# Kernel optimization log

Measured on AMD Instinct MI355X. Metric: run time of the kernel, lower is better.

Reference implementation:

```python
import jax, jax.numpy as jnp
import numpy as np

NUM_HEADS = 2
NUM_POINTS = 8
EMBED_DIM = 128


def conv2d(x, w, b, pad):
    # x: [B,C,H,W], w: [O,I,kh,kw]
    y = jax.lax.conv_general_dilated(
        x, w, window_strides=(1, 1), padding=[(pad, pad), (pad, pad)],
        dimension_numbers=('NCHW', 'OIHW', 'NCHW'))
    return y + b[None, :, None, None]


def grid_sample_bilinear(img, g):
    # img: [C,H,W]; g: [Ho,Wo,2] in [-1,1], (x, y) order; align_corners=False, zero padding
    C, H, W = img.shape
    x = ((g[..., 0] + 1.0) * W - 1.0) * 0.5
    y = ((g[..., 1] + 1.0) * H - 1.0) * 0.5
    x0 = jnp.floor(x); y0 = jnp.floor(y)
    x1 = x0 + 1.0; y1 = y0 + 1.0
    wx = x - x0; wy = y - y0

    def gather(yi, xi):
        valid = (xi >= 0) & (xi < W) & (yi >= 0) & (yi < H)
        xi_c = jnp.clip(xi, 0, W - 1).astype(jnp.int32)
        yi_c = jnp.clip(yi, 0, H - 1).astype(jnp.int32)
        v = img[:, yi_c, xi_c]  # [C,Ho,Wo]
        return v * valid[None].astype(img.dtype)

    out = (gather(y0, x0) * ((1 - wy) * (1 - wx))[None]
           + gather(y0, x1) * ((1 - wy) * wx)[None]
           + gather(y1, x0) * (wy * (1 - wx))[None]
           + gather(y1, x1) * (wy * wx)[None])
    return out  # [C,Ho,Wo]


def setup_inputs() -> dict:
    key = jax.random.key(0)
    ks = jax.random.split(key, 6)
    B, C, H, W = 8, EMBED_DIM, 96, 96
    query = jax.random.normal(ks[0], (B, C, H, W), dtype=jnp.float32)
    value = jax.random.normal(ks[1], (B, C, H, W), dtype=jnp.float32)
    reference_points = jax.random.uniform(ks[2], (B, H, W, NUM_HEADS, NUM_POINTS, 2), dtype=jnp.float32)
    attn_w = jax.random.normal(ks[3], (NUM_HEADS * NUM_POINTS, C, 3, 3), dtype=jnp.float32) * 0.05
    attn_b = jnp.zeros((NUM_HEADS * NUM_POINTS,), dtype=jnp.float32)
    proj_w = jax.random.normal(ks[4], (C, C, 1, 1), dtype=jnp.float32) * 0.05
    proj_b = jnp.zeros((C,), dtype=jnp.float32)
    return {"query": query, "value": value, "reference_points": reference_points,
            "attn_w": attn_w, "attn_b": attn_b, "proj_w": proj_w, "proj_b": proj_b}


def reference(query, value, reference_points, attn_w, attn_b, proj_w, proj_b):
    B, C, H, W = query.shape
    nh, npts = NUM_HEADS, NUM_POINTS
    hd = C // nh

    # attention weights: Conv2d(C, nh*np, 3, pad=1) -> softmax over points
    attn = conv2d(query, attn_w, attn_b, 1).reshape(B, nh, npts, H, W)
    attn = jax.nn.softmax(attn, axis=2)

    # grid: [B,H,W,nh,np,2] in [0,1] -> [-1,1] -> [B*nh, np, H, W, 2]
    grid = reference_points * 2.0 - 1.0
    grid = jnp.transpose(grid, (0, 3, 4, 1, 2, 5)).reshape(B * nh, npts, H, W, 2)

    # value per head: [B*nh, hd, H, W]
    val = value.reshape(B, nh, hd, H, W).reshape(B * nh, hd, H, W)

    # sample each point from the shared per-head value map (no materialized expand)
    sample_pts = jax.vmap(grid_sample_bilinear, in_axes=(None, 0))   # over points
    sampled = jax.vmap(sample_pts, in_axes=(0, 0))(val, grid)        # [B*nh, np, hd, H, W]
    sampled = sampled.reshape(B, nh, npts, hd, H, W)

    # weighted sum over points
    weighted = jnp.einsum('bnphw,bnpdhw->bndhw', attn, sampled).reshape(B, C, H, W)

    return conv2d(weighted, proj_w, proj_b, 0)
```

## Files before the change

### kernel.cpp

```cpp
#include <hip/hip_runtime.h>
#include <hip/hip_bf16.h>

#define BB 8
#define CC 128
#define HH 96
#define WW 96
#define HWH (HH*WW)
#define NH 2
#define NP 8
#define PW 98
#define PHW (PW*PW)

typedef __attribute__((ext_vector_type(8))) short short8;
typedef __attribute__((ext_vector_type(4))) float f32x4;

__device__ __forceinline__ float bf_lo(unsigned u) { return __uint_as_float(u << 16); }
__device__ __forceinline__ float bf_hi(unsigned u) { return __uint_as_float(u & 0xffff0000u); }

__global__ __launch_bounds__(256) void prep_w_kernel(
    const float* __restrict__ aw, const float* __restrict__ pw,
    __hip_bfloat16* __restrict__ wtb, float* __restrict__ pwT) {
  int t = blockIdx.x * 256 + threadIdx.x;
  for (int idx = t; idx < 9 * 16 * 16 * 8; idx += gridDim.x * 256) {
    int j = idx & 7;
    int o = (idx >> 3) & 15;
    int g = (idx >> 7) & 15;
    int k = idx >> 11;
    int c = g * 8 + j;
    wtb[idx] = __float2bfloat16(aw[o * 1152 + c * 9 + k]);
  }
  for (int idx = t; idx < 128 * 128; idx += gridDim.x * 256) {
    int co = idx & 127;
    int ci = idx >> 7;
    pwT[ci * 128 + co] = pw[co * 128 + ci];
  }
}

__global__ __launch_bounds__(256) void transpose_cl_kernel(
    const float* __restrict__ value, const float* __restrict__ query,
    __hip_bfloat16* __restrict__ val_t, __hip_bfloat16* __restrict__ q_pad) {
  __shared__ float tile[64][65];
  int blk = blockIdx.x;
  int mode = blk / 2304;
  int r = blk % 2304;
  int ptile = r % 144;
  int bn = r / 144;
  int b = bn >> 1, n = bn & 1;
  int pix0 = ptile * 64;
  int t = threadIdx.x;
  int lane = t & 63;
  int row4 = t >> 6;

  const float* srcp = (mode ? query : value) + ((size_t)(b * CC + n * 64)) * HWH + pix0;
#pragma unroll
  for (int i = 0; i < 16; ++i) {
    int c = i * 4 + row4;
    tile[c][lane] = srcp[(size_t)c * HWH + lane];
  }
  __syncthreads();

  int d2 = t & 31;
  int ph = t >> 5;
  if (mode == 0) {
    __hip_bfloat16* dst = val_t + ((size_t)bn * HWH + pix0) * 64;
#pragma unroll
    for (int i = 0; i < 8; ++i) {
      int p = i * 8 + ph;
      __hip_bfloat162 v;
      v.x = __float2bfloat16(tile[d2 * 2][p]);
      v.y = __float2bfloat16(tile[d2 * 2 + 1][p]);
      *reinterpret_cast<__hip_bfloat162*>(dst + (size_t)p * 64 + d2 * 2) = v;
    }
  } else {
#pragma unroll
    for (int i = 0; i < 8; ++i) {
      int p = i * 8 + ph;
      int gp = pix0 + p;
      int h = gp / WW, w = gp - h * WW;
      __hip_bfloat162 v;
      v.x = __float2bfloat16(tile[d2 * 2][p]);
      v.y = __float2bfloat16(tile[d2 * 2 + 1][p]);
      size_t off = ((size_t)b * PHW + (size_t)(h + 1) * PW + (w + 1)) * 128 + n * 64 + d2 * 2;
      *reinterpret_cast<__hip_bfloat162*>(q_pad + off) = v;
    }
  }
}

__global__ __launch_bounds__(256) void attn_conv_mfma2(
    const __hip_bfloat16* __restrict__ q_pad, const __hip_bfloat16* __restrict__ wtb_,
    const float* __restrict__ bias, float* __restrict__ attn_out) {
  int t = threadIdx.x;
  int l = t & 63;
  int bid = blockIdx.x;
  int sbid = (bid & 7) * 144 + (bid >> 3);
  int tid = __builtin_amdgcn_readfirstlane(sbid * 4 + (t >> 6));
  int b = tid / 576;
  int rem = tid % 576;
  int h = rem / 6;
  int w0 = (rem % 6) * 16;

  const char* qb = (const char*)q_pad;
  const char* wb = (const char*)wtb_;

  int pxbase = b * PHW + (h + 1) * PW + (w0 + 1);
  int lb  = (l & 15) * 256 + (l >> 4) * 16;
  int wlb = (l >> 4) * 256 + (l & 15) * 16;

  float bias_o = bias[l & 15];
  f32x4 acc0 = {bias_o, bias_o, bias_o, bias_o};
  f32x4 acc1 = {0.f, 0.f, 0.f, 0.f};

#pragma unroll
  for (int k = 0; k < 9; ++k) {
    int dy = k / 3 - 1, dx = (k % 3) - 1;
    const char* abase = qb + ((size_t)pxbase + dy * PW + dx) * 256 + lb;
    const char* bbase = wb + k * 4096 + wlb;
#pragma unroll
    for (int c4 = 0; c4 < 4; ++c4) {
      short8 a = *(const short8*)(abase + c4 * 64);
      short8 bf = *(const short8*)(bbase + c4 * 1024);
      if (k & 1)
        acc1 = __builtin_amdgcn_mfma_f32_16x16x32_bf16(a, bf, acc1, 0, 0, 0);
      else
        acc0 = __builtin_amdgcn_mfma_f32_16x16x32_bf16(a, bf, acc0, 0, 0, 0);
    }
  }

  int o = l & 15;
  size_t row0 = (size_t)b * HWH + (size_t)h * 96 + w0 + (l >> 4) * 4;
#pragma unroll
  for (int r = 0; r < 4; ++r) {
    float vv = acc0[r] + acc1[r];
    float mx = vv;
    mx = fmaxf(mx, __shfl_xor(mx, 1, 64));
    mx = fmaxf(mx, __shfl_xor(mx, 2, 64));
    mx = fmaxf(mx, __shfl_xor(mx, 4, 64));
    float e = __expf(vv - mx);
    float s = e;
    s += __shfl_xor(s, 1, 64);
    s += __shfl_xor(s, 2, 64);
    s += __shfl_xor(s, 4, 64);
    attn_out[(row0 + r) * 16 + o] = e / s;
  }
}

__global__ __launch_bounds__(256) void sample_kernel(
    const __hip_bfloat16* __restrict__ val_t, const float* __restrict__ attn,
    const float* __restrict__ refp, __hip_bfloat16* __restrict__ weighted) {
  int t = threadIdx.x;
  int lane = t & 63;
  int sub = lane >> 4;
  int lq = lane & 15;
  int bid = blockIdx.x;
  int sbid = (bid & 7) * 1152 + (bid >> 3);
  int unit = (sbid * 4 + (t >> 6)) * 4 + sub;
  int bn = unit / HWH;
  int pix = unit - bn * HWH;
  int bq = bn >> 1, n = bn & 1;

  const float* ap = attn + ((size_t)bq * HWH + pix) * 16 + n * 8;
  const float* rp = refp + (((size_t)bq * HWH + pix) * NH + n) * 16;
  const __hip_bfloat16* vb = val_t + (size_t)bn * (HWH * 64);

  float4 a0 = *(const float4*)(ap);
  float4 a1 = *(const float4*)(ap + 4);
  float4 r0 = *(const float4*)(rp);
  float4 r1 = *(const float4*)(rp + 4);
  float4 r2 = *(const float4*)(rp + 8);
  float4 r3 = *(const float4*)(rp + 12);
  float aa[8] = {a0.x, a0.y, a0.z, a0.w, a1.x, a1.y, a1.z, a1.w};
  float rr[16] = {r0.x, r0.y, r0.z, r0.w, r1.x, r1.y, r1.z, r1.w,
                  r2.x, r2.y, r2.z, r2.w, r3.x, r3.y, r3.z, r3.w};

  float acc0 = 0.f, acc1 = 0.f, acc2 = 0.f, acc3 = 0.f;
  int lq4 = lq * 4;
#pragma unroll
  for (int p = 0; p < 8; ++p) {
    float a = aa[p];
    float x = rr[p * 2 + 0] * (float)WW - 0.5f;
    float y = rr[p * 2 + 1] * (float)HH - 0.5f;
    float x0f = floorf(x), y0f = floorf(y);
    float wx = x - x0f, wy = y - y0f;
    int x0 = (int)x0f, y0 = (int)y0f;

    float ay0 = a * (1.f - wy);  ay0 = (y0 >= 0)      ? ay0 : 0.f;
    float ay1 = a * wy;          ay1 = (y0 < HH - 1)  ? ay1 : 0.f;
    float bx0 = 1.f - wx;        bx0 = (x0 >= 0)      ? bx0 : 0.f;
    float bx1 = wx;              bx1 = (x0 < WW - 1)  ? bx1 : 0.f;

    int xc0 = max(x0, 0), xc1 = min(x0 + 1, WW - 1);
    int yc0 = max(y0, 0), yc1 = min(y0 + 1, HH - 1);

    int r0o = yc0 * (WW * 64);
    int r1o = yc1 * (WW * 64);
    int c0o = xc0 * 64 + lq4;
    int c1o = xc1 * 64 + lq4;

    const uint2* p00 = (const uint2*)(vb + (r0o + c0o));
    const uint2* p01 = (const uint2*)(vb + (r0o + c1o));
    const uint2* p10 = (const uint2*)(vb + (r1o + c0o));
    const uint2* p11 = (const uint2*)(vb + (r1o + c1o));
    uint2 u00 = *p00, u01 = *p01, u10 = *p10, u11 = *p11;

    float w00 = ay0 * bx0, w01 = ay0 * bx1, w10 = ay1 * bx0, w11 = ay1 * bx1;

    acc0 = fmaf(bf_lo(u00.x), w00, acc0);
    acc1 = fmaf(bf_hi(u00.x), w00, acc1);
    acc2 = fmaf(bf_lo(u00.y), w00, acc2);
    acc3 = fmaf(bf_hi(u00.y), w00, acc3);

    acc0 = fmaf(bf_lo(u01.x), w01, acc0);
    acc1 = fmaf(bf_hi(u01.x), w01, acc1);
    acc2 = fmaf(bf_lo(u01.y), w01, acc2);
    acc3 = fmaf(bf_hi(u01.y), w01, acc3);

    acc0 = fmaf(bf_lo(u10.x), w10, acc0);
    acc1 = fmaf(bf_hi(u10.x), w10, acc1);
    acc2 = fmaf(bf_lo(u10.y), w10, acc2);
    acc3 = fmaf(bf_hi(u10.y), w10, acc3);

    acc0 = fmaf(bf_lo(u11.x), w11, acc0);
    acc1 = fmaf(bf_hi(u11.x), w11, acc1);
    acc2 = fmaf(bf_lo(u11.y), w11, acc2);
    acc3 = fmaf(bf_hi(u11.y), w11, acc3);
  }

  ushort4 outv;
  __hip_bfloat16 h0 = __float2bfloat16(acc0);
  __hip_bfloat16 h1 = __float2bfloat16(acc1);
  __hip_bfloat16 h2 = __float2bfloat16(acc2);
  __hip_bfloat16 h3 = __float2bfloat16(acc3);
  outv.x = *(unsigned short*)&h0;
  outv.y = *(unsigned short*)&h1;
  outv.z = *(unsigned short*)&h2;
  outv.w = *(unsigned short*)&h3;
  *(ushort4*)(weighted + ((size_t)bq * HWH + pix) * 128 + n * 64 + lq4) = outv;
}

__global__ __launch_bounds__(256) void proj_kernel(
    const __hip_bfloat16* __restrict__ weighted, const float* __restrict__ pwT,
    const float* __restrict__ pb, float* __restrict__ out) {
  __shared__ float A[64][129];
  int t = threadIdx.x;
  int pix0 = blockIdx.x * 64;

  const ushort4* src = reinterpret_cast<const ushort4*>(weighted + (size_t)pix0 * 128);
#pragma unroll
  for (int i = 0; i < 8; ++i) {
    int idx = i * 256 + t;
    ushort4 v = src[idx];
    int row = idx >> 5;
    int col = (idx & 31) * 4;
    A[row][col + 0] = __bfloat162float(*reinterpret_cast<__hip_bfloat16*>(&v.x));
    A[row][col + 1] = __bfloat162float(*reinterpret_cast<__hip_bfloat16*>(&v.y));
    A[row][col + 2] = __bfloat162float(*reinterpret_cast<__hip_bfloat16*>(&v.z));
    A[row][col + 3] = __bfloat162float(*reinterpret_cast<__hip_bfloat16*>(&v.w));
  }
  __syncthreads();

  int lane = t & 63;
  int g = __builtin_amdgcn_readfirstlane(t >> 6);

  float acc[32];
  const float* pbg = pb + g * 32;
#pragma unroll
  for (int j = 0; j < 32; ++j) acc[j] = pbg[j];

  const float* pwt_g = pwT + g * 32;
  for (int ci = 0; ci < 128; ++ci) {
    float a = A[lane][ci];
    const float* row = pwt_g + (size_t)ci * 128;
#pragma unroll
    for (int j = 0; j < 32; ++j) acc[j] = fmaf(a, row[j], acc[j]);
  }

  int gp = pix0 + lane;
  int b = gp / HWH;
  int pixl = gp % HWH;
  float* ob = out + ((size_t)b * CC + g * 32) * HWH + pixl;
#pragma unroll
  for (int j = 0; j < 32; ++j) ob[(size_t)j * HWH] = acc[j];
}

extern "C" void kernel_launch(void* const* d_in, const int* in_sizes, int n_in,
                              void* d_out, int out_size, void* d_ws, size_t ws_size,
                              hipStream_t stream) {
  const float* query = (const float*)d_in[0];
  const float* value = (const float*)d_in[1];
  const float* refp  = (const float*)d_in[2];
  const float* aw    = (const float*)d_in[3];
  const float* ab    = (const float*)d_in[4];
  const float* pw    = (const float*)d_in[5];
  const float* pb    = (const float*)d_in[6];
  float* out = (float*)d_out;

  char* ws = (char*)d_ws;
  __hip_bfloat16* wtb      = (__hip_bfloat16*)(ws);
  float* pwT               = (float*)(ws + 40960);
  float* attn_sm           = (float*)(ws + 106496);
  __hip_bfloat16* val_t    = (__hip_bfloat16*)(ws + 4825088);
  __hip_bfloat16* q_pad    = (__hip_bfloat16*)(ws + 23699456);
  __hip_bfloat16* weighted = (__hip_bfloat16*)(ws + 23699456);

  hipMemsetAsync(q_pad, 0, (size_t)BB * PHW * 128 * 2, stream);
  prep_w_kernel<<<72, 256, 0, stream>>>(aw, pw, wtb, pwT);
  transpose_cl_kernel<<<4608, 256, 0, stream>>>(value, query, val_t, q_pad);
  attn_conv_mfma2<<<1152, 256, 0, stream>>>(q_pad, wtb, ab, attn_sm);
  sample_kernel<<<9216, 256, 0, stream>>>(val_t, attn_sm, refp, weighted);
  proj_kernel<<<(BB * HWH) / 64, 256, 0, stream>>>(weighted, pwT, pb, out);
}
```

Measured before the change: 256.9 us.

## Replace scalar FP32 output projection with bf16 MFMA kernel

```diff
diff --git a/kernel.cpp b/kernel.cpp
--- a/kernel.cpp
+++ b/kernel.cpp
@@ -19,7 +19,7 @@
 
 __global__ __launch_bounds__(256) void prep_w_kernel(
     const float* __restrict__ aw, const float* __restrict__ pw,
-    __hip_bfloat16* __restrict__ wtb, float* __restrict__ pwT) {
+    __hip_bfloat16* __restrict__ wtb, __hip_bfloat16* __restrict__ pwb) {
   int t = blockIdx.x * 256 + threadIdx.x;
   for (int idx = t; idx < 9 * 16 * 16 * 8; idx += gridDim.x * 256) {
     int j = idx & 7;
@@ -30,9 +30,7 @@
     wtb[idx] = __float2bfloat16(aw[o * 1152 + c * 9 + k]);
   }
   for (int idx = t; idx < 128 * 128; idx += gridDim.x * 256) {
-    int co = idx & 127;
-    int ci = idx >> 7;
-    pwT[ci * 128 + co] = pw[co * 128 + ci];
+    pwb[idx] = __float2bfloat16(pw[idx]);
   }
 }
 
@@ -196,11 +194,10 @@
     int c0o = xc0 * 64 + lq4;
     int c1o = xc1 * 64 + lq4;
 
-    const uint2* p00 = (const uint2*)(vb + (r0o + c0o));
-    const uint2* p01 = (const uint2*)(vb + (r0o + c1o));
-    const uint2* p10 = (const uint2*)(vb + (r1o + c0o));
-    const uint2* p11 = (const uint2*)(vb + (r1o + c1o));
-    uint2 u00 = *p00, u01 = *p01, u10 = *p10, u11 = *p11;
+    uint2 u00 = *(const uint2*)(vb + (r0o + c0o));
+    uint2 u01 = *(const uint2*)(vb + (r0o + c1o));
+    uint2 u10 = *(const uint2*)(vb + (r1o + c0o));
+    uint2 u11 = *(const uint2*)(vb + (r1o + c1o));
 
     float w00 = ay0 * bx0, w01 = ay0 * bx1, w10 = ay1 * bx0, w11 = ay1 * bx1;
 
@@ -237,49 +234,44 @@
   *(ushort4*)(weighted + ((size_t)bq * HWH + pix) * 128 + n * 64 + lq4) = outv;
 }
 
-__global__ __launch_bounds__(256) void proj_kernel(
-    const __hip_bfloat16* __restrict__ weighted, const float* __restrict__ pwT,
+__global__ __launch_bounds__(256) void proj_mfma_kernel(
+    const __hip_bfloat16* __restrict__ weighted, const __hip_bfloat16* __restrict__ pwb,
     const float* __restrict__ pb, float* __restrict__ out) {
-  __shared__ float A[64][129];
   int t = threadIdx.x;
-  int pix0 = blockIdx.x * 64;
-
-  const ushort4* src = reinterpret_cast<const ushort4*>(weighted + (size_t)pix0 * 128);
-#pragma unroll
-  for (int i = 0; i < 8; ++i) {
-    int idx = i * 256 + t;
-    ushort4 v = src[idx];
-    int row = idx >> 5;
-    int col = (idx & 31) * 4;
-    A[row][col + 0] = __bfloat162float(*reinterpret_cast<__hip_bfloat16*>(&v.x));
-    A[row][col + 1] = __bfloat162float(*reinterpret_cast<__hip_bfloat16*>(&v.y));
-    A[row][col + 2] = __bfloat162float(*reinterpret_cast<__hip_bfloat16*>(&v.z));
-    A[row][col + 3] = __bfloat162float(*reinterpret_cast<__hip_bfloat16*>(&v.w));
-  }
-  __syncthreads();
-
-  int lane = t & 63;
-  int g = __builtin_amdgcn_readfirstlane(t >> 6);
-
-  float acc[32];
-  const float* pbg = pb + g * 32;
-#pragma unroll
-  for (int j = 0; j < 32; ++j) acc[j] = pbg[j];
-
-  const float* pwt_g = pwT + g * 32;
-  for (int ci = 0; ci < 128; ++ci) {
-    float a = A[lane][ci];
-    const float* row = pwt_g + (size_t)ci * 128;
-#pragma unroll
-    for (int j = 0; j < 32; ++j) acc[j] = fmaf(a, row[j], acc[j]);
-  }
-
-  int gp = pix0 + lane;
-  int b = gp / HWH;
-  int pixl = gp % HWH;
-  float* ob = out + ((size_t)b * CC + g * 32) * HWH + pixl;
-#pragma unroll
-  for (int j = 0; j < 32; ++j) ob[(size_t)j * HWH] = acc[j];
+  int l = t & 63;
+  int wv = t >> 6;
+  int px0 = (blockIdx.x * 4 + wv) * 16;
+  int b = px0 / HWH;
+  int pixl0 = px0 - b * HWH;
+
+  const short* wgt = (const short*)pwb;
+  const short* act = (const short*)weighted;
+
+  short8 bfrag[4];
+#pragma unroll
+  for (int kk = 0; kk < 4; ++kk)
+    bfrag[kk] = *(const short8*)(act + ((size_t)(px0 + (l & 15)) << 7) + kk * 32 + (l >> 4) * 8);
+
+  int arow = (l & 15) << 7;
+  int kofs = (l >> 4) * 8;
+
+  float* ob0 = out + (size_t)b * CC * HWH + pixl0 + (l & 15);
+  int corow = (l >> 4) * 4;
+
+#pragma unroll 2
+  for (int ct = 0; ct < 8; ++ct) {
+    float4 pb4 = *(const float4*)(pb + ct * 16 + corow);
+    f32x4 acc = {pb4.x, pb4.y, pb4.z, pb4.w};
+#pragma unroll
+    for (int kk = 0; kk < 4; ++kk) {
+      short8 afrag = *(const short8*)(wgt + ((ct * 16) << 7) + arow + kk * 32 + kofs);
+      acc = __builtin_amdgcn_mfma_f32_16x16x32_bf16(afrag, bfrag[kk], acc, 0, 0, 0);
+    }
+    float* obc = ob0 + (size_t)(ct * 16 + corow) * HWH;
+#pragma unroll
+    for (int r = 0; r < 4; ++r)
+      obc[(size_t)r * HWH] = acc[r];
+  }
 }
 
 extern "C" void kernel_launch(void* const* d_in, const int* in_sizes, int n_in,
@@ -296,16 +288,16 @@
 
   char* ws = (char*)d_ws;
   __hip_bfloat16* wtb      = (__hip_bfloat16*)(ws);
-  float* pwT               = (float*)(ws + 40960);
-  float* attn_sm           = (float*)(ws + 106496);
-  __hip_bfloat16* val_t    = (__hip_bfloat16*)(ws + 4825088);
-  __hip_bfloat16* q_pad    = (__hip_bfloat16*)(ws + 23699456);
-  __hip_bfloat16* weighted = (__hip_bfloat16*)(ws + 23699456);
+  __hip_bfloat16* pwb      = (__hip_bfloat16*)(ws + 40960);
+  float* attn_sm           = (float*)(ws + 73728);
+  __hip_bfloat16* val_t    = (__hip_bfloat16*)(ws + 4792320);
+  __hip_bfloat16* q_pad    = (__hip_bfloat16*)(ws + 23666688);
+  __hip_bfloat16* weighted = (__hip_bfloat16*)(ws + 23666688);
 
   hipMemsetAsync(q_pad, 0, (size_t)BB * PHW * 128 * 2, stream);
-  prep_w_kernel<<<72, 256, 0, stream>>>(aw, pw, wtb, pwT);
+  prep_w_kernel<<<72, 256, 0, stream>>>(aw, pw, wtb, pwb);
   transpose_cl_kernel<<<4608, 256, 0, stream>>>(value, query, val_t, q_pad);
   attn_conv_mfma2<<<1152, 256, 0, stream>>>(q_pad, wtb, ab, attn_sm);
   sample_kernel<<<9216, 256, 0, stream>>>(val_t, attn_sm, refp, weighted);
-  proj_kernel<<<(BB * HWH) / 64, 256, 0, stream>>>(weighted, pwT, pb, out);
-}
+  proj_mfma_kernel<<<(BB * HWH) / 64, 256, 0, stream>>>(weighted, pwb, pb, out);
+}
```

Measured after the change: 234.7 us. 1.09x faster.
